# Kernel optimization log

Measured on AMD Instinct MI355X. Metric: run time of the kernel, lower is better.

Reference implementation:

```python
import jax, jax.numpy as jnp
import numpy as np

NEG_INF = -1e5  # module default neg_inf


def setup_inputs() -> dict:
    key = jax.random.key(0)
    k1, k2 = jax.random.split(key)
    B, T, V, U = 64, 1000, 512, 256
    log_posteriors = jax.random.normal(k1, (B, T, V), dtype=jnp.float32)
    lens = jnp.ones((B,), dtype=jnp.float32)
    phns = jax.random.randint(k2, (B, U), 0, V)
    phn_lens = jnp.ones((B,), dtype=jnp.float32)
    return {"log_posteriors": log_posteriors, "lens": lens, "phns": phns, "phn_lens": phn_lens}


def _forward_scores(log_posteriors, lens, phns, phn_lens):
    B, T, V = log_posteriors.shape
    U = phns.shape[1]
    lens_abs = jnp.round(lens * T).astype(jnp.int32)
    phn_lens_abs = jnp.round(phn_lens * U).astype(jnp.int32)

    # --- pi: all initial mass on first phoneme ---
    pi = jnp.full((B, U), NEG_INF, dtype=jnp.float32).at[:, 0].set(0.0)

    # --- transition log-probs: self-loop + advance-by-one, length-masked, row log_softmax ---
    base = jnp.eye(U, dtype=jnp.float32) + jnp.eye(U, k=1, dtype=jnp.float32)  # (U,U)
    m = jnp.arange(U)[None, :] < phn_lens_abs[:, None]  # (B,U) valid-phoneme mask
    m2 = m[:, :, None] & m[:, None, :]  # (B,U,U)
    masked = base[None, :, :] * m2.astype(jnp.float32)
    logits = jnp.where(masked == 1.0, 1.0, -jnp.inf)
    trans = jax.nn.log_softmax(logits, axis=2)
    # nan (all -inf rows) and -inf -> neg_inf, as in the torch module
    trans = jnp.where(jnp.isnan(trans) | jnp.isinf(trans), NEG_INF, trans)  # (B,U,U)

    # --- emissions rearranged to phoneme-sequence order: (B, U, T) as (T, B, U) scan seq ---
    mask_t = jnp.arange(T)[None, :] < lens_abs[:, None]  # (B,T)
    ep = jnp.where(mask_t[:, :, None], log_posteriors, NEG_INF)
    idx = jnp.broadcast_to(phns[:, None, :], (B, T, U))
    gathered = jnp.take_along_axis(ep, idx, axis=2)  # (B,T,U)
    emiss = jnp.where(m[:, None, :], gathered, NEG_INF)  # (B,T,U)
    emiss_seq = jnp.swapaxes(emiss, 0, 1)  # (T,B,U)

    # --- forward DP: alpha[t,i] = logsumexp_j(trans[j,i] + alpha[t-1,j]) + emiss[t,i] ---
    transT = jnp.swapaxes(trans, 1, 2)  # (B, to, from)
    alpha0 = pi + emiss_seq[0]  # (B,U), unmasked as in torch (masked entries ~2*neg_inf anyway)

    def step(alpha, e_t):
        x = jax.nn.logsumexp(transT + alpha[:, None, :], axis=2)  # batch_log_matvecmul
        alpha_new = jnp.where(m, x + e_t, NEG_INF)
        return alpha_new, None

    alphaT, _ = jax.lax.scan(step, alpha0, emiss_seq[1:])
    return jax.nn.logsumexp(alphaT, axis=1)  # (B,) log-likelihoods


def reference(log_posteriors, lens, phns, phn_lens):
    return _forward_scores(log_posteriors, lens, phns, phn_lens)
```

## Files before the change

### kernel.cpp

```cpp
#include <hip/hip_runtime.h>
#include <math.h>

constexpr int Bc = 64;
constexpr int Tc = 1000;
constexpr int Vc = 512;
constexpr int Uc = 256;
constexpr int CH = 50;
constexpr int NCH = Tc / CH;
constexpr int PW = 7;
constexpr int SLOTS = 4;

constexpr int GW = 2;
constexpr int GNR = 10;
constexpr int GROWS = GW * GNR;
constexpr int GBLK = Tc / GROWS;

#define NEG_INF_F (-100000.0f)
#define LOG2E_F 1.44269504088896340736f
#define LN2_F 0.69314718055994530942f
#define DEAD_F (-1.0e9f)
#define EBIAS 30

__device__ __forceinline__ float fexp2(float x) {
#if __has_builtin(__builtin_amdgcn_exp2f)
    return __builtin_amdgcn_exp2f(x);
#else
    return __expf(x * LN2_F);
#endif
}
__device__ __forceinline__ float flog2(float x) {
#if __has_builtin(__builtin_amdgcn_logf)
    return __builtin_amdgcn_logf(x);
#else
    return __logf(x) * LOG2E_F;
#endif
}

__device__ __forceinline__ float l2add(float x, float y) {
    float m = fmaxf(x, y);
    float p = fexp2(-fabsf(x - y));
    return m + flog2(1.0f + p);
}

__device__ __forceinline__ float waveshr1(float x, float lane0val) {
    return __int_as_float(__builtin_amdgcn_update_dpp(
        __float_as_int(lane0val), __float_as_int(x),
        0x138 , 0xF, 0xF, false));
}
__device__ __forceinline__ int waveshr1_i(int x) {
    return __builtin_amdgcn_update_dpp(x, x, 0x138, 0xF, 0xF, false);
}

__device__ __forceinline__ void hmm_step_f32(float rr[4], const float4 ev,
                                             float sc_d) {
    float nb0 = waveshr1(rr[3], 0.0f) * sc_d;
    float s0 = rr[0] + nb0;
    float s1 = rr[1] + rr[0];
    float s2 = rr[2] + rr[1];
    float s3 = rr[3] + rr[2];
    rr[0] = s0 * ev.x;
    rr[1] = s1 * ev.y;
    rr[2] = s2 * ev.z;
    rr[3] = s3 * ev.w;
}

__device__ __forceinline__ void hmm_step(float rr[4], const float4 ev) {
    float nb0 = waveshr1(rr[3], DEAD_F);
    float e[4] = {ev.x, ev.y, ev.z, ev.w};
    float nb[4] = {nb0, rr[0], rr[1], rr[2]};
#pragma unroll
    for (int c = 0; c < 4; ++c) {
        float x = rr[c], y = nb[c];
        float m = fmaxf(x, y);
        float p = fexp2(-fabsf(x - y));
        float me = m + e[c];
        rr[c] = me + flog2(1.0f + p);
    }
}

__device__ __forceinline__ void dma16(const float* gsrc, float* lds, int lane) {
    typedef const __attribute__((address_space(1))) unsigned int* gp_t;
    typedef __attribute__((address_space(3))) unsigned int* lp_t;
    __builtin_amdgcn_global_load_lds((gp_t)(const void*)(gsrc + 4 * lane),
                                     (lp_t)(void*)lds, 16, 0, 0);
}

__global__ __launch_bounds__(128, 2) void gather_kernel(
    const float* __restrict__ lp, const float* __restrict__ lens,
    const int* __restrict__ phns, const float* __restrict__ phn_lens,
    float* __restrict__ el) {
    __shared__ float stage[GW][GNR][Vc];
    const int b = blockIdx.x;
    const int t0 = blockIdx.y * GROWS;
    const int tid = threadIdx.x;
    const int wave = tid >> 6;
    const int lane = tid & 63;
    const int Tv = (int)rintf(lens[b] * (float)Tc);
    const int Uv = (int)rintf(phn_lens[b] * (float)Uc);
    const float* lpb = lp + (size_t)b * Tc * Vc;
    float* elb = el + ((size_t)b * Tc + t0) * Uc;

    int col[4];
    float off[4];
    bool pv[4];
    int4 cc = *(const int4*)(phns + (size_t)b * Uc + 4 * lane);
    int c4[4] = {cc.x, cc.y, cc.z, cc.w};
#pragma unroll
    for (int c = 0; c < 4; ++c) {
        int v = c4[c];
        v = v < 0 ? 0 : (v > Vc - 1 ? Vc - 1 : v);
        col[c] = v;
        int i = 4 * lane + c;
        pv[c] = (i < Uv);
        off[c] = (i == Uv - 1) ? 0.0f : -1.0f;
    }

    float* stw = &stage[wave][0][0];
#pragma unroll
    for (int j = 0; j < GNR; ++j) {
        int r = wave + j * GW;
        const float* gsrc = lpb + (size_t)(t0 + r) * Vc;
        float* st = stw + j * Vc;
        dma16(gsrc, st, lane);
        dma16(gsrc + 256, st + 256, lane);
    }

    auto do_rows = [&](int j0) {
#pragma unroll
        for (int j = j0; j < j0 + GNR / 2; ++j) {
            int r = wave + j * GW;
            const bool tv = (t0 + r) < Tv;
            const float* st = stw + j * Vc;
            float ev[4];
#pragma unroll
            for (int c = 0; c < 4; ++c) {
                float e = st[col[c]];
                ev[c] = (pv[c] && tv) ? fexp2(fmaf(e, LOG2E_F, off[c])) : 0.0f;
            }
            *(float4*)(elb + (size_t)r * Uc + 4 * lane) =
                make_float4(ev[0], ev[1], ev[2], ev[3]);
        }
    };

    __builtin_amdgcn_s_waitcnt(0x0f7A);
    do_rows(0);
    __builtin_amdgcn_s_waitcnt(0x0f70);
    do_rows(GNR / 2);
}

__global__ __launch_bounds__(64, 1) void scan_kernel(
    const float* __restrict__ el, const float* __restrict__ phn_lens,
    float* __restrict__ out) {
    __shared__ float ebuf[2][CH][Uc];
    const int b = blockIdx.x;
    const int lane = threadIdx.x & 63;
    const int Uv = (int)rintf(phn_lens[b] * (float)Uc);
    const float* eb = el + (size_t)b * Tc * Uc;
    float rr[4];
    int e = 0;
    float sc_d = 1.0f;

    auto fill = [&](int k) {
        const float* src = eb + (size_t)k * CH * Uc;
        float* dst = &ebuf[k & 1][0][0];
#pragma unroll 5
        for (int r = 0; r < CH; ++r)
            dma16(src + (size_t)r * Uc, dst + r * Uc, lane);
    };

    auto renorm = [&]() {
        float m = fmaxf(fmaxf(rr[0], rr[1]), fmaxf(rr[2], rr[3]));
        int ep_old = waveshr1_i(e);
        bool nz = (m > 0.0f);
        int ik = ((__float_as_int(m) >> 23) & 255) - 127 - EBIAS;
        ik = ik < -96 ? -96 : (ik > 96 ? 96 : ik);
        const float sc = __int_as_float((127 - ik) << 23);
        rr[0] *= sc; rr[1] *= sc; rr[2] *= sc; rr[3] *= sc;
        e = nz ? (e + ik) : ep_old;
        int ep = waveshr1_i(e);
        int d = ep - e;
        int dc = d < -126 ? -126 : (d > 127 ? 127 : d);
        float sd = __int_as_float((127 + dc) << 23);
        sc_d = (d < -126) ? 0.0f : sd;
    };

    auto consume = [&](int k) {
        const float4* base = (const float4*)&ebuf[k & 1][0][0] + lane;
        int r = 0;
        if (k == 0) {
            float4 e0 = base[0];
            float ea[4] = {e0.x, e0.y, e0.z, e0.w};
#pragma unroll
            for (int c = 0; c < 4; ++c)
                rr[c] = (4 * lane + c == 0) ? ea[c] : 0.0f;
            r = 1;
        }
        float4 q0, q1, q2, q3;
        if (r + 0 < CH) q0 = base[(r + 0) * 64];
        if (r + 1 < CH) q1 = base[(r + 1) * 64];
        if (r + 2 < CH) q2 = base[(r + 2) * 64];
        if (r + 3 < CH) q3 = base[(r + 3) * 64];
        while (r + 4 <= CH) {
            float4 e0 = q0, e1 = q1, e2v = q2, e3 = q3;
            if (r + 4 < CH) q0 = base[(r + 4) * 64];
            if (r + 5 < CH) q1 = base[(r + 5) * 64];
            if (r + 6 < CH) q2 = base[(r + 6) * 64];
            if (r + 7 < CH) q3 = base[(r + 7) * 64];
            hmm_step_f32(rr, e0, sc_d);
            hmm_step_f32(rr, e1, sc_d);
            hmm_step_f32(rr, e2v, sc_d);
            hmm_step_f32(rr, e3, sc_d);
            renorm();
            r += 4;
        }
        bool tail = false;
        if (r + 0 < CH) { hmm_step_f32(rr, q0, sc_d); tail = true; }
        if (r + 1 < CH) { hmm_step_f32(rr, q1, sc_d); }
        if (r + 2 < CH) { hmm_step_f32(rr, q2, sc_d); }
        if (tail) renorm();
    };

    fill(0);
    __builtin_amdgcn_s_waitcnt(0x0f70);
    for (int k = 0; k < NCH; ++k) {
        if (k + 1 < NCH) fill(k + 1);
        consume(k);
        __builtin_amdgcn_s_waitcnt(0x0f70);
    }

    float a = 0.0f;
#pragma unroll
    for (int c = 0; c < 4; ++c)
        a += rr[c] * ((4 * lane + c == Uv - 1) ? 1.0f : 2.0f);
    float v = (a > 0.0f) ? (flog2(a) + (float)e) : -1.0e30f;
#pragma unroll
    for (int o = 32; o >= 1; o >>= 1) {
        float t = __shfl_xor(v, o, 64);
        v = l2add(v, t);
    }
    if (lane == 0) out[b] = v * LN2_F;
}

__global__ __launch_bounds__(512, 1) void fused_hmm_kernel(
    const float* __restrict__ lp, const float* __restrict__ lens,
    const int* __restrict__ phns, const float* __restrict__ phn_lens,
    float* __restrict__ out) {
    __shared__ float ebuf[2][CH][Uc];
    __shared__ float stage[PW][SLOTS][Vc];
    const int b = blockIdx.x;
    const int tid = threadIdx.x;
    const int wave = tid >> 6;
    const int lane = tid & 63;
    const int Tv = (int)rintf(lens[b] * (float)Tc);
    const int Uv = (int)rintf(phn_lens[b] * (float)Uc);
    const float* lpb = lp + (size_t)b * Tc * Vc;

    int col[4];
    float off[4];
    bool pv[4];
    float rr[4];

    if (wave > 0) {
        int4 cc = *(const int4*)(phns + (size_t)b * Uc + 4 * lane);
        int c4[4] = {cc.x, cc.y, cc.z, cc.w};
#pragma unroll
        for (int c = 0; c < 4; ++c) {
            int v = c4[c];
            v = v < 0 ? 0 : (v > Vc - 1 ? Vc - 1 : v);
            col[c] = v;
            int i = 4 * lane + c;
            pv[c] = (i < Uv);
            off[c] = (i == Uv - 1) ? 0.0f : -1.0f;
        }
    }

    auto fill = [&](int k) {
        float* dst = &ebuf[k & 1][0][0];
        const int tb = k * CH;
        const int r0 = wave - 1;
        float* stw = &stage[wave - 1][0][0];
#pragma unroll
        for (int half = 0; half < 2; ++half) {
#pragma unroll
            for (int jj = 0; jj < SLOTS; ++jj) {
                int r = r0 + (half * SLOTS + jj) * PW;
                if (r < CH) {
                    const float* gsrc = lpb + (size_t)(tb + r) * Vc;
                    float* st = stw + jj * Vc;
                    dma16(gsrc, st, lane);
                    dma16(gsrc + 256, st + 256, lane);
                }
            }
            __builtin_amdgcn_s_waitcnt(0x0f70);
#pragma unroll
            for (int jj = 0; jj < SLOTS; ++jj) {
                int r = r0 + (half * SLOTS + jj) * PW;
                if (r < CH) {
                    const bool tv = (tb + r) < Tv;
                    const float* st = stw + jj * Vc;
                    float ev[4];
#pragma unroll
                    for (int c = 0; c < 4; ++c) {
                        float e = st[col[c]];
                        ev[c] = (pv[c] && tv) ? fmaf(e, LOG2E_F, off[c])
                                              : (NEG_INF_F * LOG2E_F + off[c]);
                    }
                    *(float4*)(dst + r * Uc + 4 * lane) =
                        make_float4(ev[0], ev[1], ev[2], ev[3]);
                }
            }
        }
    };

    auto consume = [&](int k) {
        const float4* base = (const float4*)&ebuf[k & 1][0][0] + lane;
        int r = 0;
        if (k == 0) {
            float4 e0 = base[0];
            float ea[4] = {e0.x, e0.y, e0.z, e0.w};
#pragma unroll
            for (int c = 0; c < 4; ++c)
                rr[c] = ((4 * lane + c == 0) ? 0.0f : DEAD_F) + ea[c];
            r = 1;
        }
        float4 q0, q1, q2, q3;
        if (r + 0 < CH) q0 = base[(r + 0) * 64];
        if (r + 1 < CH) q1 = base[(r + 1) * 64];
        if (r + 2 < CH) q2 = base[(r + 2) * 64];
        if (r + 3 < CH) q3 = base[(r + 3) * 64];
        while (r + 4 <= CH) {
            float4 e0 = q0, e1 = q1, e2 = q2, e3 = q3;
            if (r + 4 < CH) q0 = base[(r + 4) * 64];
            if (r + 5 < CH) q1 = base[(r + 5) * 64];
            if (r + 6 < CH) q2 = base[(r + 6) * 64];
            if (r + 7 < CH) q3 = base[(r + 7) * 64];
            hmm_step(rr, e0);
            hmm_step(rr, e1);
            hmm_step(rr, e2);
            hmm_step(rr, e3);
            r += 4;
        }
        if (r + 0 < CH) hmm_step(rr, q0);
        if (r + 1 < CH) hmm_step(rr, q1);
        if (r + 2 < CH) hmm_step(rr, q2);
    };

    if (wave > 0) fill(0);
    __syncthreads();
    for (int k = 0; k < NCH; ++k) {
        if (wave > 0) {
            if (k + 1 < NCH) fill(k + 1);
        } else {
            consume(k);
        }
        __syncthreads();
    }

    if (wave == 0) {
        float a[4];
#pragma unroll
        for (int c = 0; c < 4; ++c)
            a[c] = rr[c] + ((4 * lane + c == Uv - 1) ? 0.0f : 1.0f);
        float r2 = l2add(l2add(a[0], a[1]), l2add(a[2], a[3]));
#pragma unroll
        for (int o = 32; o >= 1; o >>= 1) {
            float t = __shfl_xor(r2, o, 64);
            r2 = l2add(r2, t);
        }
        if (lane == 0) out[b] = r2 * LN2_F;
    }
}

extern "C" void kernel_launch(void* const* d_in, const int* in_sizes, int n_in,
                              void* d_out, int out_size, void* d_ws, size_t ws_size,
                              hipStream_t stream) {
    const float* lp = (const float*)d_in[0];
    const float* lens = (const float*)d_in[1];
    const int* phns = (const int*)d_in[2];
    const float* phn_lens = (const float*)d_in[3];
    float* out = (float*)d_out;
    (void)in_sizes; (void)n_in; (void)out_size;

    const size_t need = (size_t)Bc * Tc * Uc * sizeof(float);
    if (d_ws != nullptr && ws_size >= need) {
        float* el = (float*)d_ws;
        gather_kernel<<<dim3(Bc, GBLK), 128, 0, stream>>>(lp, lens, phns,
                                                          phn_lens, el);
        scan_kernel<<<Bc, 64, 0, stream>>>(el, phn_lens, out);
    } else {
        fused_hmm_kernel<<<Bc, 512, 0, stream>>>(lp, lens, phns, phn_lens, out);
    }
}
```

Before: 277.1 us.

## Store gathered emissions as bf16 and triple-buffer scan prefetch

```diff
diff --git a/kernel.cpp b/kernel.cpp
--- a/kernel.cpp
+++ b/kernel.cpp
@@ -15,11 +15,15 @@
 constexpr int GROWS = GW * GNR;
 constexpr int GBLK = Tc / GROWS;
 
+constexpr int FPC = CH * Uc * 2 / 1024;
+
 #define NEG_INF_F (-100000.0f)
 #define LOG2E_F 1.44269504088896340736f
 #define LN2_F 0.69314718055994530942f
 #define DEAD_F (-1.0e9f)
 #define EBIAS 30
+
+#define WAITVM(n) __builtin_amdgcn_s_waitcnt(((n) & 15) | (((n) >> 4) << 14) | 0x0f70)
 
 __device__ __forceinline__ float fexp2(float x) {
 #if __has_builtin(__builtin_amdgcn_exp2f)
@@ -49,6 +53,21 @@
 }
 __device__ __forceinline__ int waveshr1_i(int x) {
     return __builtin_amdgcn_update_dpp(x, x, 0x138, 0xF, 0xF, false);
+}
+
+__device__ __forceinline__ float4 unbf(uint2 u) {
+    float4 f;
+    f.x = __uint_as_float(u.x << 16);
+    f.y = __uint_as_float(u.x & 0xffff0000u);
+    f.z = __uint_as_float(u.y << 16);
+    f.w = __uint_as_float(u.y & 0xffff0000u);
+    return f;
+}
+__device__ __forceinline__ unsigned int bfpack(float a, float b) {
+    unsigned int xa = __float_as_uint(a), xb = __float_as_uint(b);
+    xa = (xa + 0x7fffu + ((xa >> 16) & 1u)) >> 16;
+    xb = (xb + 0x7fffu + ((xb >> 16) & 1u)) & 0xffff0000u;
+    return xa | xb;
 }
 
 __device__ __forceinline__ void hmm_step_f32(float rr[4], const float4 ev,
@@ -78,17 +97,17 @@
     }
 }
 
-__device__ __forceinline__ void dma16(const float* gsrc, float* lds, int lane) {
+__device__ __forceinline__ void dma16(const void* gsrc, void* lds, int lane) {
     typedef const __attribute__((address_space(1))) unsigned int* gp_t;
     typedef __attribute__((address_space(3))) unsigned int* lp_t;
-    __builtin_amdgcn_global_load_lds((gp_t)(const void*)(gsrc + 4 * lane),
-                                     (lp_t)(void*)lds, 16, 0, 0);
+    __builtin_amdgcn_global_load_lds((gp_t)((const char*)gsrc + 16 * lane),
+                                     (lp_t)lds, 16, 0, 0);
 }
 
 __global__ __launch_bounds__(128, 2) void gather_kernel(
     const float* __restrict__ lp, const float* __restrict__ lens,
     const int* __restrict__ phns, const float* __restrict__ phn_lens,
-    float* __restrict__ el) {
+    unsigned short* __restrict__ el) {
     __shared__ float stage[GW][GNR][Vc];
     const int b = blockIdx.x;
     const int t0 = blockIdx.y * GROWS;
@@ -98,7 +117,7 @@
     const int Tv = (int)rintf(lens[b] * (float)Tc);
     const int Uv = (int)rintf(phn_lens[b] * (float)Uc);
     const float* lpb = lp + (size_t)b * Tc * Vc;
-    float* elb = el + ((size_t)b * Tc + t0) * Uc;
+    unsigned short* elb = el + ((size_t)b * Tc + t0) * Uc;
 
     int col[4];
     float off[4];
@@ -137,35 +156,37 @@
                 float e = st[col[c]];
                 ev[c] = (pv[c] && tv) ? fexp2(fmaf(e, LOG2E_F, off[c])) : 0.0f;
             }
-            *(float4*)(elb + (size_t)r * Uc + 4 * lane) =
-                make_float4(ev[0], ev[1], ev[2], ev[3]);
-        }
-    };
-
-    __builtin_amdgcn_s_waitcnt(0x0f7A);
+            uint2 pk;
+            pk.x = bfpack(ev[0], ev[1]);
+            pk.y = bfpack(ev[2], ev[3]);
+            *(uint2*)((char*)elb + (size_t)r * Uc * 2 + 8 * lane) = pk;
+        }
+    };
+
+    WAITVM(10);
     do_rows(0);
-    __builtin_amdgcn_s_waitcnt(0x0f70);
+    WAITVM(0);
     do_rows(GNR / 2);
 }
 
 __global__ __launch_bounds__(64, 1) void scan_kernel(
-    const float* __restrict__ el, const float* __restrict__ phn_lens,
+    const unsigned short* __restrict__ el, const float* __restrict__ phn_lens,
     float* __restrict__ out) {
-    __shared__ float ebuf[2][CH][Uc];
+    __shared__ unsigned short ebuf[3][CH][Uc];
     const int b = blockIdx.x;
     const int lane = threadIdx.x & 63;
     const int Uv = (int)rintf(phn_lens[b] * (float)Uc);
-    const float* eb = el + (size_t)b * Tc * Uc;
+    const char* eb = (const char*)(el + (size_t)b * Tc * Uc);
     float rr[4];
     int e = 0;
     float sc_d = 1.0f;
 
     auto fill = [&](int k) {
-        const float* src = eb + (size_t)k * CH * Uc;
-        float* dst = &ebuf[k & 1][0][0];
-#pragma unroll 5
-        for (int r = 0; r < CH; ++r)
-            dma16(src + (size_t)r * Uc, dst + r * Uc, lane);
+        const char* src = eb + (size_t)k * CH * Uc * 2;
+        char* dst = (char*)&ebuf[k % 3][0][0];
+#pragma unroll
+        for (int i = 0; i < FPC; ++i)
+            dma16(src + i * 1024, dst + i * 1024, lane);
     };
 
     auto renorm = [&]() {
@@ -185,47 +206,51 @@
     };
 
     auto consume = [&](int k) {
-        const float4* base = (const float4*)&ebuf[k & 1][0][0] + lane;
+        const uint2* base = (const uint2*)&ebuf[k % 3][0][0] + lane;
         int r = 0;
         if (k == 0) {
-            float4 e0 = base[0];
+            float4 e0 = unbf(base[0]);
             float ea[4] = {e0.x, e0.y, e0.z, e0.w};
 #pragma unroll
             for (int c = 0; c < 4; ++c)
                 rr[c] = (4 * lane + c == 0) ? ea[c] : 0.0f;
             r = 1;
         }
-        float4 q0, q1, q2, q3;
+        uint2 q0, q1, q2, q3;
         if (r + 0 < CH) q0 = base[(r + 0) * 64];
         if (r + 1 < CH) q1 = base[(r + 1) * 64];
         if (r + 2 < CH) q2 = base[(r + 2) * 64];
         if (r + 3 < CH) q3 = base[(r + 3) * 64];
         while (r + 4 <= CH) {
-            float4 e0 = q0, e1 = q1, e2v = q2, e3 = q3;
+            uint2 e0 = q0, e1 = q1, e2v = q2, e3 = q3;
             if (r + 4 < CH) q0 = base[(r + 4) * 64];
             if (r + 5 < CH) q1 = base[(r + 5) * 64];
             if (r + 6 < CH) q2 = base[(r + 6) * 64];
             if (r + 7 < CH) q3 = base[(r + 7) * 64];
-            hmm_step_f32(rr, e0, sc_d);
-            hmm_step_f32(rr, e1, sc_d);
-            hmm_step_f32(rr, e2v, sc_d);
-            hmm_step_f32(rr, e3, sc_d);
+            hmm_step_f32(rr, unbf(e0), sc_d);
+            hmm_step_f32(rr, unbf(e1), sc_d);
+            hmm_step_f32(rr, unbf(e2v), sc_d);
+            hmm_step_f32(rr, unbf(e3), sc_d);
             renorm();
             r += 4;
         }
         bool tail = false;
-        if (r + 0 < CH) { hmm_step_f32(rr, q0, sc_d); tail = true; }
-        if (r + 1 < CH) { hmm_step_f32(rr, q1, sc_d); }
-        if (r + 2 < CH) { hmm_step_f32(rr, q2, sc_d); }
+        if (r + 0 < CH) { hmm_step_f32(rr, unbf(q0), sc_d); tail = true; }
+        if (r + 1 < CH) { hmm_step_f32(rr, unbf(q1), sc_d); }
+        if (r + 2 < CH) { hmm_step_f32(rr, unbf(q2), sc_d); }
         if (tail) renorm();
     };
 
+    WAITVM(0);
     fill(0);
-    __builtin_amdgcn_s_waitcnt(0x0f70);
+    fill(1);
+    fill(2);
     for (int k = 0; k < NCH; ++k) {
-        if (k + 1 < NCH) fill(k + 1);
+        if (k + 2 < NCH) WAITVM(2 * FPC);
+        else if (k + 1 < NCH) WAITVM(FPC);
+        else WAITVM(0);
         consume(k);
-        __builtin_amdgcn_s_waitcnt(0x0f70);
+        if (k + 3 < NCH) fill(k + 3);
     }
 
     float a = 0.0f;
@@ -291,7 +316,7 @@
                     dma16(gsrc + 256, st + 256, lane);
                 }
             }
-            __builtin_amdgcn_s_waitcnt(0x0f70);
+            WAITVM(0);
 #pragma unroll
             for (int jj = 0; jj < SLOTS; ++jj) {
                 int r = r0 + (half * SLOTS + jj) * PW;
@@ -381,9 +406,9 @@
     float* out = (float*)d_out;
     (void)in_sizes; (void)n_in; (void)out_size;
 
-    const size_t need = (size_t)Bc * Tc * Uc * sizeof(float);
+    const size_t need = (size_t)Bc * Tc * Uc * 2;
     if (d_ws != nullptr && ws_size >= need) {
-        float* el = (float*)d_ws;
+        unsigned short* el = (unsigned short*)d_ws;
         gather_kernel<<<dim3(Bc, GBLK), 128, 0, stream>>>(lp, lens, phns,
                                                           phn_lens, el);
         scan_kernel<<<Bc, 64, 0, stream>>>(el, phn_lens, out);
```

New measurement: 255.2 us. -7.9%, faster.
